# Kernel optimization log

Hardware: AMD Instinct MI355X
Metric: run time of the kernel (lower is better)

## Reference

```python
import jax, jax.numpy as jnp
import numpy as np


def _gru_dir(x, wih, whh, bih, bhh):
    # x: [B, T, Din]; torch GRU gate order is (r, z, n)
    H = whh.shape[-1]
    def step(h, xt):
        gi = xt @ wih.T + bih            # [B, 3H]
        gh = h @ whh.T + bhh             # [B, 3H]
        i_r, i_z, i_n = jnp.split(gi, 3, axis=-1)
        h_r, h_z, h_n = jnp.split(gh, 3, axis=-1)
        r = jax.nn.sigmoid(i_r + h_r)
        z = jax.nn.sigmoid(i_z + h_z)
        n = jnp.tanh(i_n + r * h_n)
        h = (1.0 - z) * n + z * h
        return h, h
    h0 = jnp.zeros((x.shape[0], H), x.dtype)
    _, ys = jax.lax.scan(step, h0, jnp.swapaxes(x, 0, 1))
    return jnp.swapaxes(ys, 0, 1)


def _bigru(x, wih, whh, bih, bhh):
    f = _gru_dir(x, wih[0], whh[0], bih[0], bhh[0])
    b = _gru_dir(x[:, ::-1], wih[1], whh[1], bih[1], bhh[1])[:, ::-1]
    return jnp.concatenate([f, b], axis=-1)


def _masked_max(h, lens):
    # max over first lens[i] timesteps; zeros when lens[i] == 0 (matches max_pool1d loop)
    T = h.shape[1]
    mask = (jnp.arange(T)[None, :] < lens[:, None])[..., None]
    pooled = jnp.max(jnp.where(mask, h, -jnp.inf), axis=1)
    return jnp.where((lens > 0)[:, None], pooled, 0.0)


def _forward(x, events, n_docs, event_tfs, sent_targets, embed,
             word_wih, word_whh, word_bih, word_bhh,
             sent_wih, sent_whh, sent_bih, sent_bhh,
             doc_wih, doc_whh, doc_bih, doc_bhh,
             ev_wih, ev_whh, ev_bih, ev_bhh,
             doc_pos_embed, sent_pos_embed,
             w_event_content, W_event_sal, event_tf, event_sent, event_bias,
             w_sent_content, W_sent_sal, w_sent_doc_pos, w_sent_pos,
             W_event_rel, b_event_rel, event_para, event_zero, sent_bias):
    S, T = x.shape
    spd = S // n_docs                  # sentences per doc (uniform doc_lens)
    eps = events.shape[0] // S         # events per sentence (uniform event_sent_lens)
    sent_lens = jnp.sum(jnp.sign(x), axis=1)
    # embed_frozen=True -> detach embedding output
    xw = jax.lax.stop_gradient(embed[x])               # [S, T, D]
    h = _bigru(xw, word_wih, word_whh, word_bih, word_bhh)  # [S, T, 2H]
    sent_vec = _masked_max(h, sent_lens)               # [S, 2H]
    # sent_RNN per doc (state resets per doc) then full-length max pool
    dh = _bigru(sent_vec.reshape(n_docs, spd, -1), sent_wih, sent_whh, sent_bih, sent_bhh)
    doc_vec = jnp.max(dh, axis=1)                      # [n_docs, 2H]
    bh = _bigru(doc_vec[None], doc_wih, doc_whh, doc_bih, doc_bhh)
    blog_vec = jnp.max(bh[0], axis=0)                  # [2H]
    # teacher_forcing=1.0 -> first-pass sent scores are the detached targets
    sent_probs0 = jax.lax.stop_gradient(sent_targets)
    # events: fixed length 4, full max pool
    eh = _bigru(jax.lax.stop_gradient(embed[events]), ev_wih, ev_whh, ev_bih, ev_bhh)
    event_vec = jnp.max(eh, axis=1)                    # [E, 2H]
    event_sum = jnp.mean(event_vec, axis=0)            # [2H] (avg pool over all events)
    abs_idx = jnp.repeat(jnp.arange(S), eps)           # event -> absolute sentence index
    ec = event_vec @ w_event_content                   # [E]
    es = jnp.einsum('ed,df,f->e', event_vec, W_event_sal, event_sum)
    event_probs = ec + event_tf[0] * event_tfs + event_bias[0] + es + event_sent[0] * sent_probs0[abs_idx]
    event_scores = jax.lax.stop_gradient(event_probs)
    # per-sentence event relevance (Bilinear with bias, dotted with detached scores)
    ev3 = event_vec.reshape(S, eps, -1)
    sc3 = event_scores.reshape(S, eps)
    sim = jnp.einsum('sd,df,sef->se', sent_vec, W_event_rel, ev3) + b_event_rel[0]
    event_rel = event_para[0] * jnp.sum(sim * sc3, axis=1)   # [S]
    doc_idx = jnp.repeat(jnp.arange(n_docs), spd)
    context = jnp.concatenate([jnp.broadcast_to(blog_vec, (S, blog_vec.shape[0])), doc_vec[doc_idx]], axis=1)  # [S, 4H]
    s_content = sent_vec @ w_sent_content
    s_sal = jnp.einsum('sd,df,sf->s', sent_vec, W_sent_sal, context)
    PD = doc_pos_embed.shape[0]
    PS = sent_pos_embed.shape[0]
    dpos = (doc_idx * PD) // n_docs                    # int(i * pos_doc_size / doc_num)
    j_idx = jnp.tile(jnp.arange(spd), n_docs)
    spos = (j_idx * PS) // spd                         # int(j * pos_sent_size / doc_lens[i])
    s_dpos = doc_pos_embed[dpos] @ w_sent_doc_pos
    s_pos = sent_pos_embed[spos] @ w_sent_pos
    sent_out = s_content + s_sal + s_dpos + s_pos + event_rel + sent_bias[0]
    return sent_out, event_probs


def setup_inputs() -> dict:
    key = jax.random.key(0)
    ks = jax.random.split(key, 40)
    V, D, H, P = 50000, 300, 256, 50
    PD, PS = 40, 30
    n_docs, spd, T, eps = 32, 32, 32, 3
    S = n_docs * spd
    E = S * eps
    def rn(k, shape, s=0.05):
        return jax.random.normal(k, shape, jnp.float32) * s
    inp = {}
    inp['x'] = jax.random.randint(ks[0], (S, T), 0, V, jnp.int32)
    inp['events'] = jax.random.randint(ks[1], (E, 4), 1, V, jnp.int32)
    inp['doc_lens'] = jnp.full((n_docs,), spd, jnp.int32)
    inp['event_doc_lens'] = jnp.full((n_docs,), spd * eps, jnp.int32)
    inp['event_sent_lens'] = jnp.full((S,), eps, jnp.int32)
    inp['event_tfs'] = jax.random.uniform(ks[2], (E,), jnp.float32)
    inp['event_targets'] = jax.random.uniform(ks[3], (E,), jnp.float32)
    inp['sent_targets'] = jax.random.uniform(ks[4], (S,), jnp.float32)
    inp['embed'] = rn(ks[5], (V, D), 0.1)
    i = 6
    for name, din in [('word', D), ('sent', 2 * H), ('doc', 2 * H), ('ev', D)]:
        inp[name + '_wih'] = rn(ks[i], (2, 3 * H, din)); i += 1
        inp[name + '_whh'] = rn(ks[i], (2, 3 * H, H)); i += 1
        inp[name + '_bih'] = rn(ks[i], (2, 3 * H)); i += 1
        inp[name + '_bhh'] = rn(ks[i], (2, 3 * H)); i += 1
    inp['doc_pos_embed'] = rn(ks[i], (PD, P), 0.1); i += 1
    inp['sent_pos_embed'] = rn(ks[i], (PS, P), 0.1); i += 1
    inp['w_event_content'] = rn(ks[i], (2 * H,)); i += 1
    inp['W_event_sal'] = rn(ks[i], (2 * H, 2 * H)); i += 1
    inp['event_tf'] = rn(ks[i], (1,)); i += 1
    inp['event_sent'] = rn(ks[i], (1,)); i += 1
    inp['event_bias'] = rn(ks[i], (1,)); i += 1
    inp['w_sent_content'] = rn(ks[i], (2 * H,)); i += 1
    inp['W_sent_sal'] = rn(ks[i], (2 * H, 4 * H)); i += 1
    inp['w_sent_doc_pos'] = rn(ks[i], (P,)); i += 1
    inp['w_sent_pos'] = rn(ks[i], (P,)); i += 1
    inp['W_event_rel'] = rn(ks[i], (2 * H, 2 * H)); i += 1
    inp['b_event_rel'] = rn(ks[i], (1,)); i += 1
    inp['event_para'] = rn(ks[i], (1,)); i += 1
    inp['event_zero'] = rn(ks[i], (1,)); i += 1
    inp['sent_bias'] = rn(ks[i], (1,)); i += 1
    return inp


def reference(x, events, doc_lens, event_doc_lens, event_sent_lens, event_tfs, event_targets, sent_targets, embed,
              word_wih, word_whh, word_bih, word_bhh,
              sent_wih, sent_whh, sent_bih, sent_bhh,
              doc_wih, doc_whh, doc_bih, doc_bhh,
              ev_wih, ev_whh, ev_bih, ev_bhh,
              doc_pos_embed, sent_pos_embed,
              w_event_content, W_event_sal, event_tf, event_sent, event_bias,
              w_sent_content, W_sent_sal, w_sent_doc_pos, w_sent_pos,
              W_event_rel, b_event_rel, event_para, event_zero, sent_bias):
    n_docs = doc_lens.shape[0]
    return _forward(x, events, n_docs, event_tfs, sent_targets, embed,
                    word_wih, word_whh, word_bih, word_bhh,
                    sent_wih, sent_whh, sent_bih, sent_bhh,
                    doc_wih, doc_whh, doc_bih, doc_bhh,
                    ev_wih, ev_whh, ev_bih, ev_bhh,
                    doc_pos_embed, sent_pos_embed,
                    w_event_content, W_event_sal, event_tf, event_sent, event_bias,
                    w_sent_content, W_sent_sal, w_sent_doc_pos, w_sent_pos,
                    W_event_rel, b_event_rel, event_para, event_zero, sent_bias)
```

## Files before the change

kernel.cpp:

```cpp
#include <hip/hip_runtime.h>
#include <hip/hip_bf16.h>
#include <math.h>

typedef __bf16 bf16_t;
typedef __bf16 bf16x8 __attribute__((ext_vector_type(8)));
typedef __bf16 bf16x4 __attribute__((ext_vector_type(4)));
typedef float  f32x4  __attribute__((ext_vector_type(4)));

#define S_TOT 1024
#define T_W   32
#define D_EMB 300
#define KP    320
#define G3    768
#define Hh    256
#define H2    512
#define E_TOT 3072
#define NCANON 33

__device__ __forceinline__ float fsigm(float x) {
  float e = __builtin_amdgcn_exp2f(x * -1.4426950408889634f);
  return __builtin_amdgcn_rcpf(1.f + e);
}
__device__ __forceinline__ float ftanh_(float x) {
  float e = __builtin_amdgcn_exp2f(x * 2.8853900817779268f);
  return 1.f - 2.f * __builtin_amdgcn_rcpf(1.f + e);
}

__global__ void k_detect(const unsigned short* __restrict__ w, int* __restrict__ flag) {
  int lane = threadIdx.x;
  int sane = 0;
  for (int i = lane; i < 256; i += 64) {
    unsigned short v = w[2 * i];
    int ex = (v >> 7) & 0xFF;
    sane += (ex >= 96 && ex <= 134) ? 1 : 0;
  }
  #pragma unroll
  for (int o = 32; o > 0; o >>= 1) sane += __shfl_down(sane, o, 64);
  if (lane == 0) flag[0] = (sane >= 128) ? 1 : 0;
}

struct Canon {
  const void* src[NCANON];
  int off[NCANON + 1];
};
__global__ void k_canon(Canon c, const int* __restrict__ flag, float* __restrict__ dst) {
  int i = blockIdx.x * 256 + threadIdx.x;
  if (i >= c.off[NCANON]) return;
  int seg = 0;
  while (c.off[seg + 1] <= i) ++seg;
  int j = i - c.off[seg];
  dst[i] = flag[0] ? (float)((const bf16_t*)c.src[seg])[j]
                   : ((const float*)c.src[seg])[j];
}

struct PrepArgs {
  const float* whh[4];   bf16_t* pk[4];
  const float* wih2[2];  bf16_t* pw2[2];
  const float* bih4[4];  const float* bhh4[4]; float* bc4[4];
  const float* tsrc[2];  float* tdst[2];
  const int* x; int* lens;
};
__global__ __launch_bounds__(256) void k_prep(PrepArgs a) {
  int b = blockIdx.x, tid = threadIdx.x;
  if (b < 768) {
    int ti = b / 192, lb = b % 192;
    int id = lb * 256 + tid;
    int lane = id & 63;
    int k0 = (id >> 6) & 7;
    int t9 = id >> 9;
    int sl = t9 % 6;
    int wb = t9 / 6;
    int wv = wb & 7;
    int dir = wb >> 3;
    int g = sl >> 1, jt = sl & 1;
    int l16 = lane & 15, quad = lane >> 4;
    int n = g * Hh + wv * 32 + jt * 16 + l16;
    const float* src = a.whh[ti] + ((size_t)dir * G3 + n) * Hh + k0 * 32 + quad * 8;
    bf16_t* dst = a.pk[ti] + (size_t)id * 8;
    #pragma unroll
    for (int i = 0; i < 8; ++i) dst[i] = (bf16_t)src[i];
  } else if (b < 1248) {
    int ti = (b - 768) / 240, lb = (b - 768) % 240;
    int id = lb * 256 + tid;
    int lane = id & 63;
    int su = id >> 6;
    int s  = su % 40;
    int n0 = (su / 40) % 12;
    int dir = su / 480;
    int j = s / 10, k0 = s % 10;
    int l16 = lane & 15, quad = lane >> 4;
    int n = n0 * 64 + j * 16 + l16;
    int c = k0 * 32 + quad * 8;
    const float* src = a.wih2[ti] + ((size_t)dir * G3 + n) * D_EMB + c;
    bf16_t* dst = a.pw2[ti] + (size_t)id * 8;
    #pragma unroll
    for (int i = 0; i < 8; ++i)
      dst[i] = (c + i < D_EMB) ? (bf16_t)src[i] : (bf16_t)0.f;
  } else if (b < 1272) {
    int ti = (b - 1248) / 6, lb = (b - 1248) % 6;
    int i = lb * 256 + tid;
    if (i < 2 * G3) {
      int c = i % G3;
      a.bc4[ti][i] = a.bih4[ti][i] + (c < 2 * Hh ? a.bhh4[ti][i] : 0.f);
    }
  } else if (b < 2808) {
    __shared__ float tile[32][33];
    int lb = b - 1272;
    int which = lb / 768;
    int r = lb % 768;
    int bx = r % 24, by = (r / 24) % 16, d = r / 384;
    const float* w = a.tsrc[which];
    float* out = a.tdst[which];
    int n0 = bx * 32, k0 = by * 32;
    int tx = tid & 31, ty = tid >> 5;
    for (int i = ty; i < 32; i += 8)
      tile[i][tx] = w[((size_t)d * G3 + n0 + i) * H2 + k0 + tx];
    __syncthreads();
    for (int i = ty; i < 32; i += 8)
      out[((size_t)d * H2 + k0 + i) * G3 + n0 + tx] = tile[tx][i];
  } else {
    int s = (b - 2808) * 256 + tid;
    if (s < S_TOT) {
      int c = 0;
      for (int t = 0; t < T_W; ++t) c += (a.x[s * T_W + t] != 0) ? 1 : 0;
      a.lens[s] = c;
    }
  }
}

__global__ __launch_bounds__(512, 1) void k_giB(
    const int* __restrict__ toks, const void* __restrict__ embed,
    const bf16_t* __restrict__ wpk_base,
    const float* __restrict__ bih_base,
    const int* __restrict__ flag, bf16_t* __restrict__ gi_base,
    size_t gi_dstride, int mbase) {
  __shared__ __align__(16) bf16_t Bt[2][20480];
  int tid = threadIdx.x;
  int wave = tid >> 6, lane = tid & 63;
  int l16 = lane & 15, quad = lane >> 4;
  int m0 = blockIdx.x * 128;
  int dir = blockIdx.y;
  int isb = flag[0];
  const bf16_t* wpk = wpk_base + (size_t)dir * 245760;
  const float*  bih = bih_base + (size_t)dir * G3;
  bf16_t* gi = gi_base + (size_t)dir * gi_dstride;

  bf16x8 ah[10], al[10];
  {
    int tok = toks[mbase + m0 + wave * 16 + l16];
    if (isb) {
      const bf16_t* er = (const bf16_t*)embed + (size_t)tok * D_EMB;
      #pragma unroll
      for (int k0 = 0; k0 < 10; ++k0) {
        int c = k0 * 32 + quad * 8;
        bf16x8 v = {};
        if (c + 8 <= D_EMB) {
          bf16x4 t0 = *(const bf16x4*)(er + c);
          bf16x4 t1 = *(const bf16x4*)(er + c + 4);
          v[0]=t0[0]; v[1]=t0[1]; v[2]=t0[2]; v[3]=t0[3];
          v[4]=t1[0]; v[5]=t1[1]; v[6]=t1[2]; v[7]=t1[3];
        } else if (c < D_EMB) {
          bf16x4 t0 = *(const bf16x4*)(er + c);
          v[0]=t0[0]; v[1]=t0[1]; v[2]=t0[2]; v[3]=t0[3];
        }
        ah[k0] = v;
        al[k0] = (bf16x8){};
      }
    } else {
      const float* er = (const float*)embed + (size_t)tok * D_EMB;
      #pragma unroll
      for (int k0 = 0; k0 < 10; ++k0) {
        int c = k0 * 32 + quad * 8;
        float v[8];
        #pragma unroll
        for (int i = 0; i < 8; ++i) v[i] = 0.f;
        if (c + 4 <= D_EMB) { float4 t = *(const float4*)(er + c);
                              v[0]=t.x; v[1]=t.y; v[2]=t.z; v[3]=t.w; }
        if (c + 8 <= D_EMB) { float4 t = *(const float4*)(er + c + 4);
                              v[4]=t.x; v[5]=t.y; v[6]=t.z; v[7]=t.w; }
        bf16x8 h, l;
        #pragma unroll
        for (int i = 0; i < 8; ++i) {
          bf16_t hv = (bf16_t)v[i];
          h[i] = hv; l[i] = (bf16_t)(v[i] - (float)hv);
        }
        ah[k0] = h; al[k0] = l;
      }
    }
  }

  bf16x8 stg[5];
  {
    const bf16_t* base = wpk + (size_t)tid * 8;
    #pragma unroll
    for (int i = 0; i < 5; ++i) stg[i] = *(const bf16x8*)(base + i * 4096);
    bf16_t* dst = &Bt[0][tid * 8];
    #pragma unroll
    for (int i = 0; i < 5; ++i) *(bf16x8*)(dst + i * 4096) = stg[i];
  }
  __syncthreads();

  for (int n0 = 0; n0 < 12; ++n0) {
    int cur = n0 & 1;
    if (n0 + 1 < 12) {
      const bf16_t* base = wpk + (size_t)(n0 + 1) * 20480 + (size_t)tid * 8;
      #pragma unroll
      for (int i = 0; i < 5; ++i) stg[i] = *(const bf16x8*)(base + i * 4096);
    }
    f32x4 acc[4];
    #pragma unroll
    for (int j = 0; j < 4; ++j) acc[j] = (f32x4){0.f, 0.f, 0.f, 0.f};
    const bf16_t* Bc = Bt[cur];
    #pragma unroll
    for (int k0 = 0; k0 < 10; ++k0) {
      bf16x8 b[4];
      #pragma unroll
      for (int j = 0; j < 4; ++j)
        b[j] = *(const bf16x8*)&Bc[((j * 10 + k0) * 64 + lane) * 8];
      if (isb) {
        #pragma unroll
        for (int j = 0; j < 4; ++j)
          acc[j] = __builtin_amdgcn_mfma_f32_16x16x32_bf16(ah[k0], b[j], acc[j], 0, 0, 0);
      } else {
        #pragma unroll
        for (int j = 0; j < 4; ++j)
          acc[j] = __builtin_amdgcn_mfma_f32_16x16x32_bf16(al[k0], b[j], acc[j], 0, 0, 0);
        #pragma unroll
        for (int j = 0; j < 4; ++j)
          acc[j] = __builtin_amdgcn_mfma_f32_16x16x32_bf16(ah[k0], b[j], acc[j], 0, 0, 0);
      }
    }
    {
      int row0 = m0 + wave * 16 + quad * 4;
      #pragma unroll
      for (int j = 0; j < 4; ++j) {
        int col = n0 * 64 + j * 16 + l16;
        float bb = bih[col];
        #pragma unroll
        for (int rr = 0; rr < 4; ++rr)
          gi[(size_t)(row0 + rr) * G3 + col] = (bf16_t)(acc[j][rr] + bb);
      }
    }
    if (n0 + 1 < 12) {
      bf16_t* dst = &Bt[cur ^ 1][tid * 8];
      #pragma unroll
      for (int i = 0; i < 5; ++i) *(bf16x8*)(dst + i * 4096) = stg[i];
      __syncthreads();
    }
  }
}

__device__ __forceinline__ void dev_sgemm(
    const float* __restrict__ A, const float* __restrict__ B,
    const float* __restrict__ bias, void* __restrict__ C,
    int M, int N, int K, int obf, int bx, int by) {
  __shared__ float As[32][65];
  __shared__ float Bs[32][65];
  int bm = bx * 64, bn = by * 64;
  int tid = threadIdx.x;
  int tx = tid & 15, ty = tid >> 4;
  float acc[4][4] = {};
  for (int k0 = 0; k0 < K; k0 += 32) {
    for (int i = tid; i < 64 * 32; i += 256) {
      int m = i >> 5, k = i & 31;
      As[k][m] = (bm + m < M) ? A[(size_t)(bm + m) * K + k0 + k] : 0.f;
    }
    for (int i = tid; i < 32 * 64; i += 256) {
      int k = i >> 6, n = i & 63;
      Bs[k][n] = B[(size_t)(k0 + k) * N + bn + n];
    }
    __syncthreads();
    #pragma unroll 8
    for (int k = 0; k < 32; ++k) {
      float a[4], b[4];
      #pragma unroll
      for (int i = 0; i < 4; ++i) a[i] = As[k][ty + i * 16];
      #pragma unroll
      for (int j = 0; j < 4; ++j) b[j] = Bs[k][tx + j * 16];
      #pragma unroll
      for (int i = 0; i < 4; ++i)
        #pragma unroll
        for (int j = 0; j < 4; ++j) acc[i][j] += a[i] * b[j];
    }
    __syncthreads();
  }
  for (int i = 0; i < 4; ++i) {
    int m = bm + ty + i * 16;
    if (m >= M) continue;
    for (int j = 0; j < 4; ++j) {
      int n = bn + tx + j * 16;
      float v = acc[i][j] + (bias ? bias[n] : 0.f);
      if (obf) ((bf16_t*)C)[(size_t)m * N + n] = (bf16_t)v;
      else     ((float*)C)[(size_t)m * N + n] = v;
    }
  }
}

__global__ __launch_bounds__(256) void k_sgemm_su(
    const float* __restrict__ sv, const float* __restrict__ wSt,
    const float* __restrict__ bcS, bf16_t* __restrict__ sgi,
    const float* __restrict__ wer, float* __restrict__ u) {
  int y = blockIdx.y;
  if (y < 12)
    dev_sgemm(sv, wSt, bcS, sgi, 1024, G3, H2, 1, blockIdx.x, y);
  else if (y < 24)
    dev_sgemm(sv, wSt + (size_t)H2 * G3, bcS + G3, sgi + (size_t)S_TOT * G3,
              1024, G3, H2, 1, blockIdx.x, y - 12);
  else
    dev_sgemm(sv, wer, nullptr, u, 1024, H2, H2, 0, blockIdx.x, y - 24);
}

__global__ __launch_bounds__(256) void k_sgemm_d(
    const float* __restrict__ dv, const float* __restrict__ wDt,
    const float* __restrict__ bcD, bf16_t* __restrict__ dgi) {
  int y = blockIdx.y;
  if (y < 12)
    dev_sgemm(dv, wDt, bcD, dgi, 32, G3, H2, 1, 0, y);
  else
    dev_sgemm(dv, wDt + (size_t)H2 * G3, bcD + G3, dgi + (size_t)32 * G3,
              32, G3, H2, 1, 0, y - 12);
}

__device__ __forceinline__ void gru_body(
    const bf16_t* __restrict__ gi, size_t gi_dstride,
    const bf16_t* __restrict__ whhP, const float* __restrict__ bhh,
    const int* __restrict__ lens, float* __restrict__ pool,
    int T, int sbase, int nsent, int sblk) {
  int dir = blockIdx.y;
  int tid = threadIdx.x;
  int wave = tid >> 6, lane = tid & 63;
  int l16 = lane & 15, quad = lane >> 4;
  const bf16_t* giD  = gi + (size_t)dir * gi_dstride;
  const float*  bhhD = bhh + (size_t)dir * G3;

  __shared__ __align__(16) bf16_t hA[2][8][16][4][8];

  bf16x8 Bf[48];
  {
    const bf16_t* Bb = whhP + (size_t)dir * G3 * Hh + (size_t)wave * 48 * 512 + lane * 8;
    #pragma unroll
    for (int s = 0; s < 48; ++s) Bf[s] = *(const bf16x8*)(Bb + s * 512);
  }
  float bhn[2];
  #pragma unroll
  for (int jt = 0; jt < 2; ++jt)
    bhn[jt] = bhhD[2 * Hh + wave * 32 + jt * 16 + l16];
  int Lm[4];
  #pragma unroll
  for (int r = 0; r < 4; ++r) {
    int sa = sblk + quad * 4 + r;
    Lm[r] = (lens && sa < nsent) ? lens[sbase + sa] : T;
  }
  float pmax[2][4], hreg[2][4];
  #pragma unroll
  for (int jt = 0; jt < 2; ++jt)
    #pragma unroll
    for (int r = 0; r < 4; ++r) { pmax[jt][r] = -1e30f; hreg[jt][r] = 0.f; }

  int t0 = dir ? (T - 1) : 0;
  long long stepoff = dir ? -(long long)G3 : (long long)G3;
  const bf16_t* rp[4];
  #pragma unroll
  for (int r = 0; r < 4; ++r)
    rp[r] = giD + ((size_t)(sblk + quad * 4 + r) * T + t0) * (size_t)G3;

  {
    bf16_t* hz = &hA[0][0][0][0][0];
    for (int i = tid; i < 8 * 16 * 4 * 8; i += 512) hz[i] = (bf16_t)0.f;
  }

  bf16_t gv[3][2][4];
  #pragma unroll
  for (int jt = 0; jt < 2; ++jt) {
    int j = wave * 32 + jt * 16 + l16;
    #pragma unroll
    for (int r = 0; r < 4; ++r) {
      gv[0][jt][r] = rp[r][j];
      gv[1][jt][r] = rp[r][Hh + j];
      gv[2][jt][r] = rp[r][2 * Hh + j];
    }
  }
  __syncthreads();

  int cur = 0;
  for (int step = 0; step < T; ++step) {
    int t = dir ? (T - 1 - step) : step;
    f32x4 C[3][2];
    #pragma unroll
    for (int g = 0; g < 3; ++g)
      #pragma unroll
      for (int jt = 0; jt < 2; ++jt) C[g][jt] = (f32x4){0.f, 0.f, 0.f, 0.f};
    #pragma unroll
    for (int k0 = 0; k0 < 8; ++k0) {
      bf16x8 a8 = *(const bf16x8*)&hA[cur][k0][l16][quad][0];
      #pragma unroll
      for (int g = 0; g < 3; ++g)
        #pragma unroll
        for (int jt = 0; jt < 2; ++jt)
          C[g][jt] = __builtin_amdgcn_mfma_f32_16x16x32_bf16(a8, Bf[(g * 2 + jt) * 8 + k0], C[g][jt], 0, 0, 0);
    }
    #pragma unroll
    for (int jt = 0; jt < 2; ++jt) {
      int q2 = jt * 2 + (l16 >> 3);
      int ii = l16 & 7;
      #pragma unroll
      for (int r = 0; r < 4; ++r) {
        int m = quad * 4 + r;
        float hp = hreg[jt][r];
        float rr = fsigm((float)gv[0][jt][r] + C[0][jt][r]);
        float zz = fsigm((float)gv[1][jt][r] + C[1][jt][r]);
        float nn = ftanh_((float)gv[2][jt][r] + rr * (C[2][jt][r] + bhn[jt]));
        float hnew = nn + zz * (hp - nn);
        hreg[jt][r] = hnew;
        hA[cur ^ 1][wave][m][q2][ii] = (bf16_t)hnew;
        if (t < Lm[r]) pmax[jt][r] = fmaxf(pmax[jt][r], hnew);
      }
    }
    #pragma unroll
    for (int r = 0; r < 4; ++r) rp[r] += stepoff;
    if (step + 1 < T) {
      #pragma unroll
      for (int jt = 0; jt < 2; ++jt) {
        int j = wave * 32 + jt * 16 + l16;
        #pragma unroll
        for (int r = 0; r < 4; ++r) {
          gv[0][jt][r] = rp[r][j];
          gv[1][jt][r] = rp[r][Hh + j];
          gv[2][jt][r] = rp[r][2 * Hh + j];
        }
      }
    }
    asm volatile("s_waitcnt lgkmcnt(0)" ::: "memory");
    __builtin_amdgcn_s_barrier();
    cur ^= 1;
  }
  #pragma unroll
  for (int jt = 0; jt < 2; ++jt) {
    int j = wave * 32 + jt * 16 + l16;
    #pragma unroll
    for (int r = 0; r < 4; ++r) {
      int sa = sblk + quad * 4 + r;
      if (sa < nsent) {
        float v = pmax[jt][r];
        if (v < -9e29f) v = 0.f;
        pool[(size_t)(sbase + sa) * H2 + dir * Hh + j] = v;
      }
    }
  }
}

__global__ __launch_bounds__(512)
__attribute__((amdgpu_waves_per_eu(2, 2)))
void k_gruM(
    const bf16_t* __restrict__ gi, size_t gi_dstride,
    const bf16_t* __restrict__ whhP, const float* __restrict__ bhh,
    const int* __restrict__ lens, float* __restrict__ pool,
    int T, int sbase, int nsent) {
  gru_body(gi, gi_dstride, whhP, bhh, lens, pool, T, sbase, nsent, blockIdx.x * 16);
}

__global__ __launch_bounds__(512)
__attribute__((amdgpu_waves_per_eu(2, 2)))
void k_gruM2(
    const bf16_t* __restrict__ giW, size_t strideW,
    const bf16_t* __restrict__ whhW, const float* __restrict__ bhhW,
    const int* __restrict__ lens, float* __restrict__ poolW, int nsentW,
    const bf16_t* __restrict__ giE, size_t strideE,
    const bf16_t* __restrict__ whhE, const float* __restrict__ bhhE,
    float* __restrict__ poolE, int nsentE, int wordBlocks) {
  if ((int)blockIdx.x < wordBlocks)
    gru_body(giW, strideW, whhW, bhhW, lens, poolW, 32, 0, nsentW,
             blockIdx.x * 16);
  else
    gru_body(giE, strideE, whhE, bhhE, nullptr, poolE, 4, 0, nsentE,
             (blockIdx.x - wordBlocks) * 16);
}

__global__ __launch_bounds__(512) void k_colsal(
    const float* __restrict__ ev, float* __restrict__ part,
    const float* __restrict__ W, const float* __restrict__ blog,
    const float* __restrict__ dv, float* __restrict__ wsal) {
  int b = blockIdx.x, t = threadIdx.x;
  if (b < 48) {
    int r0 = b * 64;
    float s = 0.f;
    for (int r = 0; r < 64; ++r) s += ev[(size_t)(r0 + r) * H2 + t];
    part[(size_t)b * H2 + t] = s;
  } else {
    int doc = b - 48;
    const float* row = W + (size_t)t * (2 * H2);
    const float* dvr = dv + (size_t)doc * H2;
    float s = 0.f;
    for (int f = 0; f < H2; ++f) s += row[f] * blog[f];
    for (int f = 0; f < H2; ++f) s += row[H2 + f] * dvr[f];
    wsal[(size_t)doc * H2 + t] = s;
  }
}

__global__ __launch_bounds__(512) void k_esumves(
    const float* __restrict__ part, const float* __restrict__ W,
    float* __restrict__ ves) {
  __shared__ float es[H2];
  int t = threadIdx.x;
  float s = 0.f;
  for (int b = 0; b < 48; ++b) s += part[(size_t)b * H2 + t];
  es[t] = s;
  __syncthreads();
  const float* row = W + (size_t)t * H2;
  float v = 0.f;
  for (int f = 0; f < H2; ++f) v += row[f] * es[f];
  ves[t] = v * (1.f / 3072.f);
}

__global__ __launch_bounds__(256) void k_eventprobs(
    const float* __restrict__ evv, const float* __restrict__ ves,
    const float* __restrict__ w_ec, const float* __restrict__ tfs,
    const float* __restrict__ st, const float* __restrict__ c_tf,
    const float* __restrict__ c_sent, const float* __restrict__ c_bias,
    const int* __restrict__ flag, float* __restrict__ probs, void* __restrict__ outp) {
  int lane = threadIdx.x & 63;
  int e = blockIdx.x * 4 + (threadIdx.x >> 6);
  const float* row = evv + (size_t)e * H2;
  float s = 0.f;
  for (int f = lane; f < H2; f += 64) s += row[f] * (w_ec[f] + ves[f]);
  #pragma unroll
  for (int o = 32; o > 0; o >>= 1) s += __shfl_down(s, o, 64);
  if (lane == 0) {
    float p = s + c_tf[0] * tfs[e] + c_bias[0] + c_sent[0] * st[e / 3];
    probs[e] = p;
    if (flag[0]) ((bf16_t*)outp)[S_TOT + e] = (bf16_t)p;
    else         ((float*)outp)[S_TOT + e] = p;
  }
}

__global__ __launch_bounds__(256) void k_sentout(
    const float* __restrict__ sv, const float* __restrict__ u,
    const float* __restrict__ evv, const float* __restrict__ probs,
    const float* __restrict__ wsal, const float* __restrict__ w_sc,
    const float* __restrict__ dpe, const float* __restrict__ spe,
    const float* __restrict__ w_sdp, const float* __restrict__ w_sp,
    const float* __restrict__ b_rel, const float* __restrict__ para,
    const float* __restrict__ sbias, const int* __restrict__ flag,
    void* __restrict__ outp) {
  int lane = threadIdx.x & 63;
  int s = blockIdx.x * 4 + (threadIdx.x >> 6);
  int doc = s >> 5, jj = s & 31;
  const float* svr = sv + (size_t)s * H2;
  const float* ur  = u + (size_t)s * H2;
  const float* wd  = wsal + (size_t)doc * H2;
  float acc = 0.f, e0 = 0.f, e1 = 0.f, e2 = 0.f;
  for (int f = lane; f < H2; f += 64) {
    float svf = svr[f], uf = ur[f];
    acc += svf * (w_sc[f] + wd[f]);
    e0 += uf * evv[(size_t)(s * 3 + 0) * H2 + f];
    e1 += uf * evv[(size_t)(s * 3 + 1) * H2 + f];
    e2 += uf * evv[(size_t)(s * 3 + 2) * H2 + f];
  }
  if (lane < 50) {
    int dpos = (doc * 40) / 32;
    int spos = (jj * 30) / 32;
    acc += dpe[dpos * 50 + lane] * w_sdp[lane] + spe[spos * 50 + lane] * w_sp[lane];
  }
  #pragma unroll
  for (int o = 32; o > 0; o >>= 1) {
    acc += __shfl_down(acc, o, 64);
    e0  += __shfl_down(e0, o, 64);
    e1  += __shfl_down(e1, o, 64);
    e2  += __shfl_down(e2, o, 64);
  }
  if (lane == 0) {
    float br = b_rel[0];
    float rel = (e0 + br) * probs[s * 3 + 0] + (e1 + br) * probs[s * 3 + 1]
              + (e2 + br) * probs[s * 3 + 2];
    float v = acc + para[0] * rel + sbias[0];
    if (flag[0]) ((bf16_t*)outp)[s] = (bf16_t)v;
    else         ((float*)outp)[s] = v;
  }
}

extern "C" void kernel_launch(void* const* d_in, const int* in_sizes, int n_in,
                              void* d_out, int out_size, void* d_ws, size_t ws_size,
                              hipStream_t stream) {
  (void)in_sizes; (void)n_in; (void)out_size;
  const int* x      = (const int*)d_in[0];
  const int* events = (const int*)d_in[1];
  const void* embed = d_in[8];

  char* ws = (char*)d_ws;
  size_t off = 0;
  auto alloc = [&](size_t bytes) -> void* {
    void* p = ws + off;
    off += (bytes + 255) & ~(size_t)255;
    return p;
  };

  static const int cidx[NCANON] = {9,10,11,12, 13,14,15,16, 17,18,19,20, 21,22,23,24,
                                   25,26,27,28,29,30,31, 32,33,34,35, 36,37,38,40, 5,7};
  static const int csz[NCANON]  = {2*G3*D_EMB, 2*G3*Hh, 2*G3, 2*G3,
                                   2*G3*H2,    2*G3*Hh, 2*G3, 2*G3,
                                   2*G3*H2,    2*G3*Hh, 2*G3, 2*G3,
                                   2*G3*D_EMB, 2*G3*Hh, 2*G3, 2*G3,
                                   40*50, 30*50, H2, H2*H2, 1, 1, 1,
                                   H2, H2*2*H2, 50, 50,
                                   H2*H2, 1, 1, 1, E_TOT, S_TOT};
  Canon cd;
  int tot = 0;
  for (int i = 0; i < NCANON; ++i) { cd.src[i] = d_in[cidx[i]]; cd.off[i] = tot; tot += csz[i]; }
  cd.off[NCANON] = tot;

  int*   flag  = (int*)alloc(256);
  float* canon = (float*)alloc((size_t)tot * 4);
  float* cptr[NCANON];
  for (int i = 0; i < NCANON; ++i) cptr[i] = canon + cd.off[i];
  float *cw_wih = cptr[0], *cw_whh = cptr[1], *cw_bih = cptr[2], *cw_bhh = cptr[3];
  float *cs_wih = cptr[4], *cs_whh = cptr[5], *cs_bih = cptr[6], *cs_bhh = cptr[7];
  float *cd_wih = cptr[8], *cd_whh = cptr[9], *cd_bih = cptr[10], *cd_bhh = cptr[11];
  float *ce_wih = cptr[12], *ce_whh = cptr[13], *ce_bih = cptr[14], *ce_bhh = cptr[15];
  float *c_dpe = cptr[16], *c_spe = cptr[17], *c_wec = cptr[18], *c_Wes = cptr[19];
  float *c_tf = cptr[20], *c_sent = cptr[21], *c_ebias = cptr[22];
  float *c_wsc = cptr[23], *c_Wss = cptr[24], *c_wsdp = cptr[25], *c_wsp = cptr[26];
  float *c_Wer = cptr[27], *c_brel = cptr[28], *c_para = cptr[29], *c_sbias = cptr[30];
  float *c_tfs = cptr[31], *c_starg = cptr[32];

  bf16_t* packW = (bf16_t*)alloc((size_t)2 * G3 * Hh * 2);
  bf16_t* packE = (bf16_t*)alloc((size_t)2 * G3 * Hh * 2);
  bf16_t* packS = (bf16_t*)alloc((size_t)2 * G3 * Hh * 2);
  bf16_t* packD = (bf16_t*)alloc((size_t)2 * G3 * Hh * 2);
  bf16_t* packGiW = (bf16_t*)alloc((size_t)2 * 12 * 40 * 64 * 8 * 2);
  bf16_t* packGiE = (bf16_t*)alloc((size_t)2 * 12 * 40 * 64 * 8 * 2);
  float*  bcW  = (float*)alloc((size_t)2 * G3 * 4);
  float*  bcE  = (float*)alloc((size_t)2 * G3 * 4);
  float*  bcS  = (float*)alloc((size_t)2 * G3 * 4);
  float*  bcD  = (float*)alloc((size_t)2 * G3 * 4);
  float*  sv   = (float*)alloc((size_t)S_TOT * H2 * 4);
  float*  evv  = (float*)alloc((size_t)E_TOT * H2 * 4);
  float*  dv   = (float*)alloc((size_t)32 * H2 * 4);
  float*  blog = (float*)alloc((size_t)H2 * 4);
  float*  wSt  = (float*)alloc((size_t)2 * H2 * G3 * 4);
  float*  wDt  = (float*)alloc((size_t)2 * H2 * G3 * 4);
  float*  u    = (float*)alloc((size_t)S_TOT * H2 * 4);
  float*  part = (float*)alloc((size_t)48 * H2 * 4);
  float*  ves  = (float*)alloc((size_t)H2 * 4);
  float*  wsal = (float*)alloc((size_t)32 * H2 * 4);
  float*  probs= (float*)alloc((size_t)E_TOT * 4);
  int*    lens = (int*)alloc((size_t)S_TOT * 4);
  bf16_t* sgi  = (bf16_t*)alloc((size_t)2 * S_TOT * G3 * 2);
  bf16_t* dgi  = (bf16_t*)alloc((size_t)2 * 32 * G3 * 2);

  size_t fixed = off;
  size_t avail = (ws_size > fixed) ? (ws_size - fixed) : 0;
  const size_t needW = (size_t)2 * 32768 * G3 * 2;
  const size_t needE = (size_t)2 * 12288 * G3 * 2;
  bf16_t* gib = (bf16_t*)(ws + fixed);

  PrepArgs pa;
  pa.whh[0]=cw_whh; pa.whh[1]=ce_whh; pa.whh[2]=cs_whh; pa.whh[3]=cd_whh;
  pa.pk[0]=packW; pa.pk[1]=packE; pa.pk[2]=packS; pa.pk[3]=packD;
  pa.wih2[0]=cw_wih; pa.wih2[1]=ce_wih; pa.pw2[0]=packGiW; pa.pw2[1]=packGiE;
  pa.bih4[0]=cw_bih; pa.bih4[1]=ce_bih; pa.bih4[2]=cs_bih; pa.bih4[3]=cd_bih;
  pa.bhh4[0]=cw_bhh; pa.bhh4[1]=ce_bhh; pa.bhh4[2]=cs_bhh; pa.bhh4[3]=cd_bhh;
  pa.bc4[0]=bcW; pa.bc4[1]=bcE; pa.bc4[2]=bcS; pa.bc4[3]=bcD;
  pa.tsrc[0]=cs_wih; pa.tsrc[1]=cd_wih; pa.tdst[0]=wSt; pa.tdst[1]=wDt;
  pa.x = x; pa.lens = lens;

  k_detect<<<1, 64, 0, stream>>>((const unsigned short*)embed, flag);
  k_canon<<<(tot + 255) / 256, 256, 0, stream>>>(cd, flag, canon);
  k_prep<<<2812, 256, 0, stream>>>(pa);

  if (avail >= needW + needE) {
    bf16_t* egib = (bf16_t*)((char*)gib + ((needW + 255) & ~(size_t)255));
    k_giB<<<dim3(256, 2), 512, 0, stream>>>(x, embed, packGiW, bcW, flag,
                                            gib, (size_t)32768 * G3, 0);
    k_giB<<<dim3(96, 2), 512, 0, stream>>>(events, embed, packGiE, bcE, flag,
                                           egib, (size_t)12288 * G3, 0);
    k_gruM2<<<dim3(64 + 192, 2), 512, 0, stream>>>(
        gib, (size_t)32768 * G3, packW, cw_bhh, lens, sv, 1024,
        egib, (size_t)12288 * G3, packE, ce_bhh, evv, 3072, 64);
  } else {
    long long rpc = (long long)(avail / ((size_t)G3 * 2 * 2));
    rpc &= ~511LL;
    if (rpc < 512) rpc = 512;
    if (rpc > 32768) rpc = 32768;
    for (long long r0 = 0; r0 < 32768; r0 += rpc) {
      long long rows = 32768 - r0; if (rows > rpc) rows = rpc;
      k_giB<<<dim3((int)(rows / 128), 2), 512, 0, stream>>>(
          x, embed, packGiW, bcW, flag, gib, (size_t)rows * G3, (int)r0);
      k_gruM<<<dim3((int)(rows / 512), 2), 512, 0, stream>>>(
          gib, (size_t)rows * G3, packW, cw_bhh, lens, sv, 32, (int)(r0 / 32),
          (int)(rows / 32));
    }
    for (long long r0 = 0; r0 < 12288; r0 += rpc) {
      long long rows = 12288 - r0; if (rows > rpc) rows = rpc;
      k_giB<<<dim3((int)(rows / 128), 2), 512, 0, stream>>>(
          events, embed, packGiE, bcE, flag, gib, (size_t)rows * G3, (int)r0);
      k_gruM<<<dim3((int)(rows / 64), 2), 512, 0, stream>>>(
          gib, (size_t)rows * G3, packE, ce_bhh, nullptr, evv, 4, (int)(r0 / 4),
          (int)(rows / 4));
    }
  }

  k_sgemm_su<<<dim3(16, 32), 256, 0, stream>>>(sv, wSt, bcS, sgi, c_Wer, u);
  k_gruM<<<dim3(2, 2), 512, 0, stream>>>(sgi, (size_t)S_TOT * G3, packS, cs_bhh,
                                         nullptr, dv, 32, 0, 32);
  k_sgemm_d<<<dim3(1, 24), 256, 0, stream>>>(dv, wDt, bcD, dgi);
  k_gruM<<<dim3(1, 2), 512, 0, stream>>>(dgi, (size_t)32 * G3, packD, cd_bhh,
                                         nullptr, blog, 32, 0, 1);
  k_colsal<<<80, 512, 0, stream>>>(evv, part, c_Wss, blog, dv, wsal);
  k_esumves<<<1, 512, 0, stream>>>(part, c_Wes, ves);
  k_eventprobs<<<768, 256, 0, stream>>>(evv, ves, c_wec, c_tfs, c_starg,
                                        c_tf, c_sent, c_ebias, flag, probs, d_out);
  k_sentout<<<256, 256, 0, stream>>>(sv, u, evv, probs, wsal, c_wsc, c_dpe, c_spe,
                                     c_wsdp, c_wsp, c_brel, c_para, c_sbias, flag, d_out);
}
```

Measured before the change: 972.6 us.

## Overlap event input-projection GEMM with word GRU recurrence in one launch

The event-token input projection (gib) now runs in the same launch as the word-level GRU recurrence, as extra blocks alongside the 64 word-GRU blocks. The event GRU recurrence moves to its own following launch. The goal is to fill idle CUs during the long, latency-bound word recurrence with the event GEMM work, instead of running that GEMM as a separate serial kernel. In exchange, the event GRU can no longer share a launch with the word GRU. The merged kernel also carries the larger shared-memory footprint and the waves_per_eu constraint of both bodies.

```diff
diff --git a/kernel.cpp b/kernel.cpp
--- a/kernel.cpp
+++ b/kernel.cpp
@@ -128,17 +128,16 @@
   }
 }
 
-__global__ __launch_bounds__(512, 1) void k_giB(
+__device__ __forceinline__ void gib_body(
     const int* __restrict__ toks, const void* __restrict__ embed,
-    const bf16_t* __restrict__ wpk_base,
-    const float* __restrict__ bih_base,
+    const bf16_t* __restrict__ wpk_base, const float* __restrict__ bih_base,
     const int* __restrict__ flag, bf16_t* __restrict__ gi_base,
-    size_t gi_dstride, int mbase) {
+    size_t gi_dstride, int mbase, int bx) {
   __shared__ __align__(16) bf16_t Bt[2][20480];
   int tid = threadIdx.x;
   int wave = tid >> 6, lane = tid & 63;
   int l16 = lane & 15, quad = lane >> 4;
-  int m0 = blockIdx.x * 128;
+  int m0 = bx * 128;
   int dir = blockIdx.y;
   int isb = flag[0];
   const bf16_t* wpk = wpk_base + (size_t)dir * 245760;
@@ -250,6 +249,15 @@
   }
 }
 
+__global__ __launch_bounds__(512, 1) void k_giB(
+    const int* __restrict__ toks, const void* __restrict__ embed,
+    const bf16_t* __restrict__ wpk_base, const float* __restrict__ bih_base,
+    const int* __restrict__ flag, bf16_t* __restrict__ gi_base,
+    size_t gi_dstride, int mbase) {
+  gib_body(toks, embed, wpk_base, bih_base, flag, gi_base, gi_dstride, mbase,
+           blockIdx.x);
+}
+
 __device__ __forceinline__ void dev_sgemm(
     const float* __restrict__ A, const float* __restrict__ B,
     const float* __restrict__ bias, void* __restrict__ C,
@@ -461,19 +469,19 @@
 
 __global__ __launch_bounds__(512)
 __attribute__((amdgpu_waves_per_eu(2, 2)))
-void k_gruM2(
+void k_wg(
     const bf16_t* __restrict__ giW, size_t strideW,
     const bf16_t* __restrict__ whhW, const float* __restrict__ bhhW,
-    const int* __restrict__ lens, float* __restrict__ poolW, int nsentW,
-    const bf16_t* __restrict__ giE, size_t strideE,
-    const bf16_t* __restrict__ whhE, const float* __restrict__ bhhE,
-    float* __restrict__ poolE, int nsentE, int wordBlocks) {
-  if ((int)blockIdx.x < wordBlocks)
-    gru_body(giW, strideW, whhW, bhhW, lens, poolW, 32, 0, nsentW,
+    const int* __restrict__ lens, float* __restrict__ poolW,
+    const int* __restrict__ etoks, const void* __restrict__ embed,
+    const bf16_t* __restrict__ wpkE, const float* __restrict__ bihE,
+    const int* __restrict__ flag, bf16_t* __restrict__ giE, size_t strideE) {
+  if ((int)blockIdx.x < 64)
+    gru_body(giW, strideW, whhW, bhhW, lens, poolW, 32, 0, 1024,
              blockIdx.x * 16);
   else
-    gru_body(giE, strideE, whhE, bhhE, nullptr, poolE, 4, 0, nsentE,
-             (blockIdx.x - wordBlocks) * 16);
+    gib_body(etoks, embed, wpkE, bihE, flag, giE, strideE, 0,
+             blockIdx.x - 64);
 }
 
 __global__ __launch_bounds__(512) void k_colsal(
@@ -671,11 +679,11 @@
     bf16_t* egib = (bf16_t*)((char*)gib + ((needW + 255) & ~(size_t)255));
     k_giB<<<dim3(256, 2), 512, 0, stream>>>(x, embed, packGiW, bcW, flag,
                                             gib, (size_t)32768 * G3, 0);
-    k_giB<<<dim3(96, 2), 512, 0, stream>>>(events, embed, packGiE, bcE, flag,
-                                           egib, (size_t)12288 * G3, 0);
-    k_gruM2<<<dim3(64 + 192, 2), 512, 0, stream>>>(
-        gib, (size_t)32768 * G3, packW, cw_bhh, lens, sv, 1024,
-        egib, (size_t)12288 * G3, packE, ce_bhh, evv, 3072, 64);
+    k_wg<<<dim3(64 + 96, 2), 512, 0, stream>>>(
+        gib, (size_t)32768 * G3, packW, cw_bhh, lens, sv,
+        events, embed, packGiE, bcE, flag, egib, (size_t)12288 * G3);
+    k_gruM<<<dim3(192, 2), 512, 0, stream>>>(
+        egib, (size_t)12288 * G3, packE, ce_bhh, nullptr, evv, 4, 0, 3072);
   } else {
     long long rpc = (long long)(avail / ((size_t)G3 * 2 * 2));
     rpc &= ~511LL;
```

Result: faster. 913.0 us (-6.1%).
